# Kernel tuning notes

Measured on AMD Instinct MI355X. Metric: run time of the kernel, lower is better.

The kernel has to match this reference:

```python
import jax, jax.numpy as jnp
import numpy as np

W_CHAMFER = 1.0
W_SMOOTH = 0.5
K_NEIGHBORS = 8


def _pairwise_sqdist(a, b):
    # a: [B,N,3], b: [B,M,3] -> [B,N,M] squared euclidean distances
    a2 = jnp.sum(a * a, axis=-1)  # [B,N]
    b2 = jnp.sum(b * b, axis=-1)  # [B,M]
    ab = jnp.einsum('bnd,bmd->bnm', a, b)  # [B,N,M]
    d2 = a2[:, :, None] + b2[:, None, :] - 2.0 * ab
    return jnp.maximum(d2, 0.0)


def _chamfer(pc1, pc2):
    d = jnp.sqrt(_pairwise_sqdist(pc1, pc2))  # [B,N,M] euclidean (matches torch.norm)
    d1 = jnp.min(d, axis=2)  # [B,N]
    d2 = jnp.min(d, axis=1)  # [B,M]
    return jnp.mean(d1) + jnp.mean(d2)


def _smoothness(pc, flow, k=K_NEIGHBORS):
    d2 = _pairwise_sqdist(pc, pc)  # [B,N,N]
    # k+1 nearest (squared dist preserves ordering); drop self (index 0)
    _, idx = jax.lax.top_k(-d2, k + 1)  # [B,N,k+1]
    idx = idx[:, :, 1:]  # [B,N,k]
    neighbor_flow = jax.vmap(lambda f, i: f[i])(flow, idx)  # [B,N,k,3]
    diff = flow[:, :, None, :] - neighbor_flow
    return jnp.mean(jnp.linalg.norm(diff, axis=-1))


def setup_inputs() -> dict:
    key = jax.random.key(0)
    k1, k2, k3 = jax.random.split(key, 3)
    B, N, M = 2, 8192, 8192
    pc1 = jax.random.normal(k1, (B, N, 3), dtype=jnp.float32)
    pc2 = jax.random.normal(k2, (B, M, 3), dtype=jnp.float32)
    pred_flow = jax.random.normal(k3, (B, N, 3), dtype=jnp.float32) * 0.1
    return {"pc1": pc1, "pc2": pc2, "pred_flow": pred_flow}


def reference(pc1, pc2, pred_flow):
    pc1_warped = pc1 + pred_flow
    l_chamfer = _chamfer(pc1_warped, pc2)
    l_smooth = _smoothness(pc1, pred_flow)
    return W_CHAMFER * l_chamfer + W_SMOOTH * l_smooth
```

## Files before the change

kernel.cpp:

```cpp
#include <hip/hip_runtime.h>

#define N_PTS 8192
#define BATCH 2
#define KNN 8
#define STILE 2048
#define PPB 16
#define CH_R 8
#define CH_SLICE 256
#define NSLICE (N_PTS / CH_SLICE)
#define CH_BLOCKS 512
#define SM_BLOCKS (N_PTS / PPB * BATCH)
#define WS_STORE_NEED (4 * 1024 * 1024)
#define OFF_MINS 0

__device__ __forceinline__ void ce(unsigned &x, unsigned &y) {
    unsigned lo = min(x, y), hi = max(x, y); x = lo; y = hi;
}

__device__ __forceinline__ void insert4(unsigned o[4], unsigned key) {
    unsigned n0 = min(o[0], key);
    unsigned n1 = max(o[0], min(o[1], key));
    unsigned n2 = max(o[1], min(o[2], key));
    unsigned n3 = max(o[2], min(o[3], key));
    o[0]=n0; o[1]=n1; o[2]=n2; o[3]=n3;
}

__device__ __forceinline__ void merge_stage8(unsigned m[8], int d) {
    unsigned p[8], c[8];
    #pragma unroll
    for (int k = 0; k < 8; ++k) p[k] = __shfl_xor(m[k], d, 64);
    #pragma unroll
    for (int k = 0; k < 8; ++k) c[k] = min(m[k], p[7-k]);
    ce(c[0],c[4]); ce(c[1],c[5]); ce(c[2],c[6]); ce(c[3],c[7]);
    ce(c[0],c[2]); ce(c[1],c[3]); ce(c[4],c[6]); ce(c[5],c[7]);
    ce(c[0],c[1]); ce(c[2],c[3]); ce(c[4],c[5]); ce(c[6],c[7]);
    #pragma unroll
    for (int k = 0; k < 8; ++k) m[k] = c[k];
}

__device__ __forceinline__ void merge64(unsigned m[8]) {
    merge_stage8(m, 1); merge_stage8(m, 2); merge_stage8(m, 4);
    merge_stage8(m, 8); merge_stage8(m, 16); merge_stage8(m, 32);
}

__global__ __launch_bounds__(256, 4) void mega_kernel(
        const float* __restrict__ pc1, const float* __restrict__ pc2,
        const float* __restrict__ flow, float* __restrict__ part,
        unsigned* __restrict__ mins, float* __restrict__ out, int store_mode) {
    __shared__ float4 sq[STILE];
    const int tid = threadIdx.x;
    const int bx = blockIdx.x;

    if (bx < CH_BLOCKS) {
        const int rt    = bx & 3;
        const int slice = (bx >> 2) & 31;
        const int z     = bx >> 7;
        const int b = z & 1, dir = z >> 1;
        const float* P1 = pc1  + (size_t)b * N_PTS * 3;
        const float* P2 = pc2  + (size_t)b * N_PTS * 3;
        const float* FL = flow + (size_t)b * N_PTS * 3;
        const int m0 = slice * CH_SLICE;

        float* sraw = (float*)(sq + 256);
        if (tid < CH_SLICE * 3 / 4) {
            float4 v;
            if (dir == 0) {
                v = ((const float4*)(P2 + (size_t)m0 * 3))[tid];
            } else {
                float4 a = ((const float4*)(P1 + (size_t)m0 * 3))[tid];
                float4 f = ((const float4*)(FL + (size_t)m0 * 3))[tid];
                v = make_float4(a.x + f.x, a.y + f.y, a.z + f.z, a.w + f.w);
            }
            ((float4*)sraw)[tid] = v;
        }

        const int i0 = rt * (256 * CH_R) + tid * CH_R;
        float mx[CH_R], my_[CH_R], mz_[CH_R], p2[CH_R], best[CH_R];
        #pragma unroll
        for (int r = 0; r < CH_R; ++r) {
            int row = i0 + r;
            float px, py, pz;
            if (dir == 0) {
                px = P1[row*3+0] + FL[row*3+0];
                py = P1[row*3+1] + FL[row*3+1];
                pz = P1[row*3+2] + FL[row*3+2];
            } else {
                px = P2[row*3+0]; py = P2[row*3+1]; pz = P2[row*3+2];
            }
            mx[r] = -2.0f * px; my_[r] = -2.0f * py; mz_[r] = -2.0f * pz;
            p2[r] = fmaf(px, px, fmaf(py, py, pz * pz));
            best[r] = __builtin_inff();
        }
        __syncthreads();
        {
            float qx = sraw[tid*3+0], qy = sraw[tid*3+1], qz = sraw[tid*3+2];
            sq[tid] = make_float4(qx, qy, qz, fmaf(qx, qx, fmaf(qy, qy, qz * qz)));
        }
        __syncthreads();

        #pragma unroll 8
        for (int jj = 0; jj < CH_SLICE; ++jj) {
            float4 q = sq[jj];
            #pragma unroll
            for (int r = 0; r < CH_R; ++r) {
                float s = fmaf(mx[r], q.x, fmaf(my_[r], q.y, fmaf(mz_[r], q.z, q.w)));
                best[r] = fminf(best[r], s);
            }
        }

        float d2v[CH_R];
        #pragma unroll
        for (int r = 0; r < CH_R; ++r) d2v[r] = fmaxf(best[r] + p2[r], 0.0f);
        if (store_mode) {
            float* dst = part + ((size_t)(z * NSLICE + slice)) * N_PTS + i0;
            *(float4*)(dst)     = make_float4(d2v[0], d2v[1], d2v[2], d2v[3]);
            *(float4*)(dst + 4) = make_float4(d2v[4], d2v[5], d2v[6], d2v[7]);
        } else {
            #pragma unroll
            for (int r = 0; r < CH_R; ++r)
                atomicMin(&mins[z * N_PTS + i0 + r], __float_as_uint(d2v[r]));
        }
    } else {
        const int s  = bx - CH_BLOCKS;
        const int b  = s >> 9;
        const int sx = s & 511;
        const int wv = tid >> 6, lane = tid & 63;
        const int i0w = sx * PPB + wv * 4;
        const float* P = pc1  + (size_t)b * N_PTS * 3;
        const float* F = flow + (size_t)b * N_PTS * 3;

        float mx[4], my[4], mz[4], p2[4], gr[4];
        unsigned thr[4];
        #pragma unroll
        for (int r = 0; r < 4; ++r) {
            int i = i0w + r;
            float px = P[i*3+0], py = P[i*3+1], pz = P[i*3+2];
            mx[r] = -2.0f * px; my[r] = -2.0f * py; mz[r] = -2.0f * pz;
            p2[r] = fmaf(px, px, fmaf(py, py, pz * pz));
            gr[r] = __builtin_inff();
            thr[r] = 0xFFFFFFFFu;
        }

        unsigned o[4][4];
        #pragma unroll
        for (int r = 0; r < 4; ++r)
            #pragma unroll
            for (int k = 0; k < 4; ++k) o[r][k] = 0xFFFFFFFFu;

        __shared__ float psum[4];

        #pragma unroll 1
        for (int tile = 0; tile < N_PTS / STILE; ++tile) {
            const int t0 = tile * STILE;
            __syncthreads();
            #pragma unroll
            for (int u = tid; u < STILE; u += 256) {
                int g = t0 + u;
                float qx = P[g*3+0], qy = P[g*3+1], qz = P[g*3+2];
                sq[u] = make_float4(qx, qy, qz, fmaf(qx, qx, fmaf(qy, qy, qz * qz)));
            }
            __syncthreads();

            if (tile == 0) {
                #pragma unroll 4
                for (int st = 0; st < STILE / 64; ++st) {
                    float4 qa = sq[st * 64 + lane];
                    int j = st * 64 + lane;
                    #pragma unroll
                    for (int r = 0; r < 4; ++r) {
                        float ss = fmaf(mx[r], qa.x, fmaf(my[r], qa.y, fmaf(mz[r], qa.z, qa.w)));
                        float d2 = fmaxf(ss + p2[r], 0.0f);
                        unsigned key = (__float_as_uint(d2) & 0xFFFFE000u) | (unsigned)j;
                        key = (j == i0w + r) ? 0xFFFFFFFFu : key;
                        insert4(o[r], key);
                    }
                }
            } else {
                #pragma unroll 4
                for (int st = 0; st < STILE / 64; ++st) {
                    float4 qa = sq[st * 64 + lane];
                    int j = t0 + st * 64 + lane;
                    float s0 = fmaf(mx[0], qa.x, fmaf(my[0], qa.y, fmaf(mz[0], qa.z, qa.w)));
                    float s1 = fmaf(mx[1], qa.x, fmaf(my[1], qa.y, fmaf(mz[1], qa.z, qa.w)));
                    float s2 = fmaf(mx[2], qa.x, fmaf(my[2], qa.y, fmaf(mz[2], qa.z, qa.w)));
                    float s3 = fmaf(mx[3], qa.x, fmaf(my[3], qa.y, fmaf(mz[3], qa.z, qa.w)));
                    if (__any(s0 <= gr[0])) {
                        float d2 = fmaxf(s0 + p2[0], 0.0f);
                        unsigned key = (__float_as_uint(d2) & 0xFFFFE000u) | (unsigned)j;
                        key = (j == i0w + 0) ? 0xFFFFFFFFu : key;
                        insert4(o[0], key);
                    }
                    if (__any(s1 <= gr[1])) {
                        float d2 = fmaxf(s1 + p2[1], 0.0f);
                        unsigned key = (__float_as_uint(d2) & 0xFFFFE000u) | (unsigned)j;
                        key = (j == i0w + 1) ? 0xFFFFFFFFu : key;
                        insert4(o[1], key);
                    }
                    if (__any(s2 <= gr[2])) {
                        float d2 = fmaxf(s2 + p2[2], 0.0f);
                        unsigned key = (__float_as_uint(d2) & 0xFFFFE000u) | (unsigned)j;
                        key = (j == i0w + 2) ? 0xFFFFFFFFu : key;
                        insert4(o[2], key);
                    }
                    if (__any(s3 <= gr[3])) {
                        float d2 = fmaxf(s3 + p2[3], 0.0f);
                        unsigned key = (__float_as_uint(d2) & 0xFFFFE000u) | (unsigned)j;
                        key = (j == i0w + 3) ? 0xFFFFFFFFu : key;
                        insert4(o[3], key);
                    }
                }
            }

            if (tile <= 2) {
                #pragma unroll
                for (int r = 0; r < 4; ++r) {
                    unsigned a = max(o[r][3], (unsigned)__shfl_xor((int)o[r][3], 1, 64));
                    a = min(a, (unsigned)__shfl_xor((int)a, 2, 64));
                    a = min(a, (unsigned)__shfl_xor((int)a, 4, 64));
                    a = min(a, (unsigned)__shfl_xor((int)a, 8, 64));
                    a = min(a, (unsigned)__shfl_xor((int)a, 16, 64));
                    a = min(a, (unsigned)__shfl_xor((int)a, 32, 64));
                    thr[r] = min(thr[r], a);
                    float thr_up = __uint_as_float((thr[r] & 0xFFFFE000u) + 0x4000u);
                    gr[r] = thr_up - p2[r];
                }
            }
        }

        unsigned fin[4][8];
        #pragma unroll
        for (int r = 0; r < 4; ++r) {
            unsigned m[8] = {o[r][0], o[r][1], o[r][2], o[r][3],
                             0xFFFFFFFFu, 0xFFFFFFFFu, 0xFFFFFFFFu, 0xFFFFFFFFu};
            merge64(m);
            #pragma unroll
            for (int k = 0; k < 8; ++k) fin[r][k] = m[k];
        }

        const int sel = lane & 31;
        unsigned key = fin[0][0];
        #pragma unroll
        for (int rr = 0; rr < 4; ++rr)
            #pragma unroll
            for (int kk = 0; kk < 8; ++kk)
                if (sel == rr * 8 + kk) key = fin[rr][kk];
        const int r = sel >> 3;
        const int i = i0w + r;
        const int j = (int)(key & (N_PTS - 1));
        float dx = F[i*3+0] - F[j*3+0];
        float dy = F[i*3+1] - F[j*3+1];
        float dz = F[i*3+2] - F[j*3+2];
        float sv = sqrtf(fmaf(dx, dx, fmaf(dy, dy, dz * dz)));
        #pragma unroll
        for (int d = 1; d < 64; d <<= 1) sv += __shfl_xor(sv, d, 64);
        if (lane == 0) psum[wv] = sv;
        __syncthreads();
        if (tid == 0) {
            atomicAdd(out, (psum[0] + psum[1] + psum[2] + psum[3]) *
                           (0.25f / ((float)BATCH * N_PTS * KNN)));
        }
    }
}

__global__ void chamfer_reduce_kernel(const unsigned* __restrict__ mins,
                                      const float* __restrict__ part,
                                      float* __restrict__ out, int store_mode) {
    int t = blockIdx.x * 256 + threadIdx.x;
    float v;
    if (store_mode) {
        int c = t >> 13, row = t & (N_PTS - 1);
        const float* p = part + ((size_t)c * NSLICE) * N_PTS + row;
        v = __builtin_inff();
        #pragma unroll 8
        for (int s = 0; s < NSLICE; ++s) v = fminf(v, p[(size_t)s * N_PTS]);
    } else {
        v = __uint_as_float(mins[t]);
    }
    float d = sqrtf(v) * (1.0f / (float)(BATCH * N_PTS));
    #pragma unroll
    for (int off = 32; off > 0; off >>= 1) d += __shfl_down(d, off, 64);
    __shared__ float wsum[4];
    int wid = threadIdx.x >> 6;
    if ((threadIdx.x & 63) == 0) wsum[wid] = d;
    __syncthreads();
    if (threadIdx.x == 0) atomicAdd(out, wsum[0] + wsum[1] + wsum[2] + wsum[3]);
}

extern "C" void kernel_launch(void* const* d_in, const int* in_sizes, int n_in,
                              void* d_out, int out_size, void* d_ws, size_t ws_size,
                              hipStream_t stream) {
    const float* pc1  = (const float*)d_in[0];
    const float* pc2  = (const float*)d_in[1];
    const float* flow = (const float*)d_in[2];
    float* out = (float*)d_out;
    float* part = (float*)d_ws;
    unsigned* mins = (unsigned*)((char*)d_ws + OFF_MINS);

    const int store_mode = (ws_size >= (size_t)WS_STORE_NEED) ? 1 : 0;

    hipMemsetAsync(out, 0, sizeof(float), stream);
    if (!store_mode) {
        hipMemsetAsync(mins, 0xFF, 4u * N_PTS * sizeof(unsigned), stream);
    }

    mega_kernel<<<dim3(CH_BLOCKS + SM_BLOCKS), 256, 0, stream>>>(
        pc1, pc2, flow, part, mins, out, store_mode);

    chamfer_reduce_kernel<<<dim3(2 * BATCH * N_PTS / 256), 256, 0, stream>>>(
        mins, part, out, store_mode);
}
```

Baseline: 151.9 us.

## Enlarge chamfer slices, tighten kNN threshold early, replace atomics with single finish kernel

```diff
diff --git a/kernel.cpp b/kernel.cpp
--- a/kernel.cpp
+++ b/kernel.cpp
@@ -4,14 +4,15 @@
 #define BATCH 2
 #define KNN 8
 #define STILE 2048
-#define PPB 16
+#define SM_PPB 16
+#define SM_BLOCKS (BATCH * N_PTS / SM_PPB)
+#define CH_SLICE 1024
 #define CH_R 8
-#define CH_SLICE 256
+#define CH_ROWG (256 * CH_R)
 #define NSLICE (N_PTS / CH_SLICE)
-#define CH_BLOCKS 512
-#define SM_BLOCKS (N_PTS / PPB * BATCH)
-#define WS_STORE_NEED (4 * 1024 * 1024)
-#define OFF_MINS 0
+#define NROWG (N_PTS / CH_ROWG)
+#define CH_BLOCKS (4 * NSLICE * NROWG)
+#define OFF_SMSUM (4 * NSLICE * N_PTS)
 
 __device__ __forceinline__ void ce(unsigned &x, unsigned &y) {
     unsigned lo = min(x, y), hi = max(x, y); x = lo; y = hi;
@@ -28,7 +29,7 @@
 __device__ __forceinline__ void merge_stage8(unsigned m[8], int d) {
     unsigned p[8], c[8];
     #pragma unroll
-    for (int k = 0; k < 8; ++k) p[k] = __shfl_xor(m[k], d, 64);
+    for (int k = 0; k < 8; ++k) p[k] = (unsigned)__shfl_xor((int)m[k], d, 64);
     #pragma unroll
     for (int k = 0; k < 8; ++k) c[k] = min(m[k], p[7-k]);
     ce(c[0],c[4]); ce(c[1],c[5]); ce(c[2],c[6]); ce(c[3],c[7]);
@@ -46,35 +47,37 @@
 __global__ __launch_bounds__(256, 4) void mega_kernel(
         const float* __restrict__ pc1, const float* __restrict__ pc2,
         const float* __restrict__ flow, float* __restrict__ part,
-        unsigned* __restrict__ mins, float* __restrict__ out, int store_mode) {
+        float* __restrict__ smsum) {
     __shared__ float4 sq[STILE];
+    __shared__ float psum[4];
     const int tid = threadIdx.x;
     const int bx = blockIdx.x;
 
     if (bx < CH_BLOCKS) {
-        const int rt    = bx & 3;
-        const int slice = (bx >> 2) & 31;
-        const int z     = bx >> 7;
+        const int z     = bx >> 5;
+        const int rowg  = bx & 3;
+        const int slice = (bx >> 2) & 7;
         const int b = z & 1, dir = z >> 1;
         const float* P1 = pc1  + (size_t)b * N_PTS * 3;
         const float* P2 = pc2  + (size_t)b * N_PTS * 3;
         const float* FL = flow + (size_t)b * N_PTS * 3;
         const int m0 = slice * CH_SLICE;
 
-        float* sraw = (float*)(sq + 256);
-        if (tid < CH_SLICE * 3 / 4) {
+        float* sraw = (float*)(sq + CH_SLICE);
+        #pragma unroll
+        for (int u = tid; u < CH_SLICE * 3 / 4; u += 256) {
             float4 v;
             if (dir == 0) {
-                v = ((const float4*)(P2 + (size_t)m0 * 3))[tid];
+                v = ((const float4*)(P2 + (size_t)m0 * 3))[u];
             } else {
-                float4 a = ((const float4*)(P1 + (size_t)m0 * 3))[tid];
-                float4 f = ((const float4*)(FL + (size_t)m0 * 3))[tid];
+                float4 a = ((const float4*)(P1 + (size_t)m0 * 3))[u];
+                float4 f = ((const float4*)(FL + (size_t)m0 * 3))[u];
                 v = make_float4(a.x + f.x, a.y + f.y, a.z + f.z, a.w + f.w);
             }
-            ((float4*)sraw)[tid] = v;
-        }
-
-        const int i0 = rt * (256 * CH_R) + tid * CH_R;
+            ((float4*)sraw)[u] = v;
+        }
+
+        const int i0 = rowg * CH_ROWG + tid * CH_R;
         float mx[CH_R], my_[CH_R], mz_[CH_R], p2[CH_R], best[CH_R];
         #pragma unroll
         for (int r = 0; r < CH_R; ++r) {
@@ -92,9 +95,10 @@
             best[r] = __builtin_inff();
         }
         __syncthreads();
-        {
-            float qx = sraw[tid*3+0], qy = sraw[tid*3+1], qz = sraw[tid*3+2];
-            sq[tid] = make_float4(qx, qy, qz, fmaf(qx, qx, fmaf(qy, qy, qz * qz)));
+        #pragma unroll
+        for (int u = tid; u < CH_SLICE; u += 256) {
+            float qx = sraw[u*3+0], qy = sraw[u*3+1], qz = sraw[u*3+2];
+            sq[u] = make_float4(qx, qy, qz, fmaf(qx, qx, fmaf(qy, qy, qz * qz)));
         }
         __syncthreads();
 
@@ -108,29 +112,22 @@
             }
         }
 
-        float d2v[CH_R];
-        #pragma unroll
-        for (int r = 0; r < CH_R; ++r) d2v[r] = fmaxf(best[r] + p2[r], 0.0f);
-        if (store_mode) {
-            float* dst = part + ((size_t)(z * NSLICE + slice)) * N_PTS + i0;
-            *(float4*)(dst)     = make_float4(d2v[0], d2v[1], d2v[2], d2v[3]);
-            *(float4*)(dst + 4) = make_float4(d2v[4], d2v[5], d2v[6], d2v[7]);
-        } else {
-            #pragma unroll
-            for (int r = 0; r < CH_R; ++r)
-                atomicMin(&mins[z * N_PTS + i0 + r], __float_as_uint(d2v[r]));
-        }
+        float* dst = part + ((size_t)(z * NSLICE + slice)) * N_PTS + i0;
+        *(float4*)(dst)     = make_float4(fmaxf(best[0]+p2[0],0.f), fmaxf(best[1]+p2[1],0.f),
+                                          fmaxf(best[2]+p2[2],0.f), fmaxf(best[3]+p2[3],0.f));
+        *(float4*)(dst + 4) = make_float4(fmaxf(best[4]+p2[4],0.f), fmaxf(best[5]+p2[5],0.f),
+                                          fmaxf(best[6]+p2[6],0.f), fmaxf(best[7]+p2[7],0.f));
     } else {
         const int s  = bx - CH_BLOCKS;
         const int b  = s >> 9;
         const int sx = s & 511;
         const int wv = tid >> 6, lane = tid & 63;
-        const int i0w = sx * PPB + wv * 4;
+        const int i0w = sx * SM_PPB + wv * 4;
         const float* P = pc1  + (size_t)b * N_PTS * 3;
         const float* F = flow + (size_t)b * N_PTS * 3;
 
         float mx[4], my[4], mz[4], p2[4], gr[4];
-        unsigned thr[4];
+        unsigned thr[4], o[4][4];
         #pragma unroll
         for (int r = 0; r < 4; ++r) {
             int i = i0w + r;
@@ -139,15 +136,52 @@
             p2[r] = fmaf(px, px, fmaf(py, py, pz * pz));
             gr[r] = __builtin_inff();
             thr[r] = 0xFFFFFFFFu;
-        }
-
-        unsigned o[4][4];
-        #pragma unroll
-        for (int r = 0; r < 4; ++r)
             #pragma unroll
             for (int k = 0; k < 4; ++k) o[r][k] = 0xFFFFFFFFu;
-
-        __shared__ float psum[4];
+        }
+
+        auto update_thr = [&]() {
+            #pragma unroll
+            for (int r = 0; r < 4; ++r) {
+                unsigned m0 = o[r][0], m1 = o[r][1], m2 = o[r][2], m3 = o[r][3];
+                #pragma unroll
+                for (int d = 1; d <= 16; d <<= 1) {
+                    unsigned q0 = (unsigned)__shfl_xor((int)m0, d, 64);
+                    unsigned q1 = (unsigned)__shfl_xor((int)m1, d, 64);
+                    unsigned q2 = (unsigned)__shfl_xor((int)m2, d, 64);
+                    unsigned q3 = (unsigned)__shfl_xor((int)m3, d, 64);
+                    unsigned c0 = min(m0, q3), c1 = min(m1, q2);
+                    unsigned c2 = min(m2, q1), c3 = min(m3, q0);
+                    ce(c0, c2); ce(c1, c3); ce(c0, c1); ce(c2, c3);
+                    m0 = c0; m1 = c1; m2 = c2; m3 = c3;
+                }
+                unsigned bound = max(m3, (unsigned)__shfl_xor((int)m3, 32, 64));
+                thr[r] = min(thr[r], bound);
+                float thr_up = __uint_as_float((thr[r] & 0xFFFFE000u) + 0x4000u);
+                gr[r] = thr_up - p2[r];
+            }
+        };
+
+        auto gated_span = [&](int t0, int st0, int st1) {
+            #pragma unroll 2
+            for (int st = st0; st < st1; ++st) {
+                float4 qa = sq[st * 64 + lane];
+                int j = t0 + st * 64 + lane;
+                float sc[4];
+                #pragma unroll
+                for (int r = 0; r < 4; ++r)
+                    sc[r] = fmaf(mx[r], qa.x, fmaf(my[r], qa.y, fmaf(mz[r], qa.z, qa.w)));
+                #pragma unroll
+                for (int r = 0; r < 4; ++r) {
+                    if (__any(sc[r] <= gr[r])) {
+                        float d2 = fmaxf(sc[r] + p2[r], 0.0f);
+                        unsigned key = (__float_as_uint(d2) & 0xFFFFE000u) | (unsigned)j;
+                        key = (j == i0w + r) ? 0xFFFFFFFFu : key;
+                        insert4(o[r], key);
+                    }
+                }
+            }
+        };
 
         #pragma unroll 1
         for (int tile = 0; tile < N_PTS / STILE; ++tile) {
@@ -163,7 +197,7 @@
 
             if (tile == 0) {
                 #pragma unroll 4
-                for (int st = 0; st < STILE / 64; ++st) {
+                for (int st = 0; st < 16; ++st) {
                     float4 qa = sq[st * 64 + lane];
                     int j = st * 64 + lane;
                     #pragma unroll
@@ -175,55 +209,12 @@
                         insert4(o[r], key);
                     }
                 }
+                update_thr();
+                gated_span(0, 16, 32);
+                update_thr();
             } else {
-                #pragma unroll 4
-                for (int st = 0; st < STILE / 64; ++st) {
-                    float4 qa = sq[st * 64 + lane];
-                    int j = t0 + st * 64 + lane;
-                    float s0 = fmaf(mx[0], qa.x, fmaf(my[0], qa.y, fmaf(mz[0], qa.z, qa.w)));
-                    float s1 = fmaf(mx[1], qa.x, fmaf(my[1], qa.y, fmaf(mz[1], qa.z, qa.w)));
-                    float s2 = fmaf(mx[2], qa.x, fmaf(my[2], qa.y, fmaf(mz[2], qa.z, qa.w)));
-                    float s3 = fmaf(mx[3], qa.x, fmaf(my[3], qa.y, fmaf(mz[3], qa.z, qa.w)));
-                    if (__any(s0 <= gr[0])) {
-                        float d2 = fmaxf(s0 + p2[0], 0.0f);
-                        unsigned key = (__float_as_uint(d2) & 0xFFFFE000u) | (unsigned)j;
-                        key = (j == i0w + 0) ? 0xFFFFFFFFu : key;
-                        insert4(o[0], key);
-                    }
-                    if (__any(s1 <= gr[1])) {
-                        float d2 = fmaxf(s1 + p2[1], 0.0f);
-                        unsigned key = (__float_as_uint(d2) & 0xFFFFE000u) | (unsigned)j;
-                        key = (j == i0w + 1) ? 0xFFFFFFFFu : key;
-                        insert4(o[1], key);
-                    }
-                    if (__any(s2 <= gr[2])) {
-                        float d2 = fmaxf(s2 + p2[2], 0.0f);
-                        unsigned key = (__float_as_uint(d2) & 0xFFFFE000u) | (unsigned)j;
-                        key = (j == i0w + 2) ? 0xFFFFFFFFu : key;
-                        insert4(o[2], key);
-                    }
-                    if (__any(s3 <= gr[3])) {
-                        float d2 = fmaxf(s3 + p2[3], 0.0f);
-                        unsigned key = (__float_as_uint(d2) & 0xFFFFE000u) | (unsigned)j;
-                        key = (j == i0w + 3) ? 0xFFFFFFFFu : key;
-                        insert4(o[3], key);
-                    }
-                }
-            }
-
-            if (tile <= 2) {
-                #pragma unroll
-                for (int r = 0; r < 4; ++r) {
-                    unsigned a = max(o[r][3], (unsigned)__shfl_xor((int)o[r][3], 1, 64));
-                    a = min(a, (unsigned)__shfl_xor((int)a, 2, 64));
-                    a = min(a, (unsigned)__shfl_xor((int)a, 4, 64));
-                    a = min(a, (unsigned)__shfl_xor((int)a, 8, 64));
-                    a = min(a, (unsigned)__shfl_xor((int)a, 16, 64));
-                    a = min(a, (unsigned)__shfl_xor((int)a, 32, 64));
-                    thr[r] = min(thr[r], a);
-                    float thr_up = __uint_as_float((thr[r] & 0xFFFFE000u) + 0x4000u);
-                    gr[r] = thr_up - p2[r];
-                }
+                gated_span(t0, 0, 32);
+                if (tile <= 2) update_thr();
             }
         }
 
@@ -236,7 +227,6 @@
             #pragma unroll
             for (int k = 0; k < 8; ++k) fin[r][k] = m[k];
         }
-
         const int sel = lane & 31;
         unsigned key = fin[0][0];
         #pragma unroll
@@ -255,35 +245,41 @@
         for (int d = 1; d < 64; d <<= 1) sv += __shfl_xor(sv, d, 64);
         if (lane == 0) psum[wv] = sv;
         __syncthreads();
-        if (tid == 0) {
-            atomicAdd(out, (psum[0] + psum[1] + psum[2] + psum[3]) *
-                           (0.25f / ((float)BATCH * N_PTS * KNN)));
-        }
+        if (tid == 0)
+            smsum[s] = psum[0] + psum[1] + psum[2] + psum[3];
     }
 }
 
-__global__ void chamfer_reduce_kernel(const unsigned* __restrict__ mins,
-                                      const float* __restrict__ part,
-                                      float* __restrict__ out, int store_mode) {
-    int t = blockIdx.x * 256 + threadIdx.x;
-    float v;
-    if (store_mode) {
-        int c = t >> 13, row = t & (N_PTS - 1);
-        const float* p = part + ((size_t)c * NSLICE) * N_PTS + row;
-        v = __builtin_inff();
-        #pragma unroll 8
-        for (int s = 0; s < NSLICE; ++s) v = fminf(v, p[(size_t)s * N_PTS]);
-    } else {
-        v = __uint_as_float(mins[t]);
+__global__ __launch_bounds__(1024) void finish_kernel(const float* __restrict__ part,
+                                                      const float* __restrict__ smsum,
+                                                      float* __restrict__ out) {
+    const int t = threadIdx.x;
+    float ch = 0.0f;
+    #pragma unroll 1
+    for (int z = 0; z < 4; ++z) {
+        #pragma unroll 2
+        for (int g = 0; g < 8; ++g) {
+            int row = g * 1024 + t;
+            const float* p = part + (size_t)z * NSLICE * N_PTS + row;
+            float v = p[0];
+            #pragma unroll
+            for (int s = 1; s < NSLICE; ++s) v = fminf(v, p[(size_t)s * N_PTS]);
+            ch += sqrtf(v);
+        }
     }
-    float d = sqrtf(v) * (1.0f / (float)(BATCH * N_PTS));
-    #pragma unroll
-    for (int off = 32; off > 0; off >>= 1) d += __shfl_down(d, off, 64);
-    __shared__ float wsum[4];
-    int wid = threadIdx.x >> 6;
-    if ((threadIdx.x & 63) == 0) wsum[wid] = d;
+    float local = ch * (1.0f / (float)(BATCH * N_PTS))
+                + smsum[t] * (0.25f / ((float)BATCH * N_PTS * KNN));
+    #pragma unroll
+    for (int d = 1; d < 64; d <<= 1) local += __shfl_xor(local, d, 64);
+    __shared__ float wsum[16];
+    if ((t & 63) == 0) wsum[t >> 6] = local;
     __syncthreads();
-    if (threadIdx.x == 0) atomicAdd(out, wsum[0] + wsum[1] + wsum[2] + wsum[3]);
+    if (t == 0) {
+        float tot = 0.0f;
+        #pragma unroll
+        for (int k = 0; k < 16; ++k) tot += wsum[k];
+        out[0] = tot;
+    }
 }
 
 extern "C" void kernel_launch(void* const* d_in, const int* in_sizes, int n_in,
@@ -293,19 +289,9 @@
     const float* pc2  = (const float*)d_in[1];
     const float* flow = (const float*)d_in[2];
     float* out = (float*)d_out;
-    float* part = (float*)d_ws;
-    unsigned* mins = (unsigned*)((char*)d_ws + OFF_MINS);
-
-    const int store_mode = (ws_size >= (size_t)WS_STORE_NEED) ? 1 : 0;
-
-    hipMemsetAsync(out, 0, sizeof(float), stream);
-    if (!store_mode) {
-        hipMemsetAsync(mins, 0xFF, 4u * N_PTS * sizeof(unsigned), stream);
-    }
-
-    mega_kernel<<<dim3(CH_BLOCKS + SM_BLOCKS), 256, 0, stream>>>(
-        pc1, pc2, flow, part, mins, out, store_mode);
-
-    chamfer_reduce_kernel<<<dim3(2 * BATCH * N_PTS / 256), 256, 0, stream>>>(
-        mins, part, out, store_mode);
-}
+    float* part  = (float*)d_ws;
+    float* smsum = (float*)d_ws + OFF_SMSUM;
+
+    mega_kernel<<<dim3(CH_BLOCKS + SM_BLOCKS), 256, 0, stream>>>(pc1, pc2, flow, part, smsum);
+    finish_kernel<<<dim3(1), 1024, 0, stream>>>(part, smsum, out);
+}
```

Result: faster. 143.8 us (-5.3%).
